# Optimization experiments

Hardware: AMD Instinct MI355X
Metric: run time of the kernel (lower is better)

Reference implementation:

```python
import jax, jax.numpy as jnp
import numpy as np

H = 64    # n_hidden
N = 1535  # input nodes; total graph nodes Nn = N + 1
B = 32    # batch
BN_EPS = 1e-5


def _p(key, shape, scale=0.05):
    return (jax.random.normal(key, shape, dtype=jnp.float32) * scale)


def setup_inputs() -> dict:
    key = jax.random.key(0)
    ks = jax.random.split(key, 32)
    inp = {
        'input_xx': jax.random.normal(ks[0], (B, N, 8), dtype=jnp.float32),
        'input_yy': jax.random.normal(ks[1], (B, N), dtype=jnp.float32),
        'output_xx': jax.random.normal(ks[2], (B, 1, 8), dtype=jnp.float32),
        # fc1: Linear(9, H); fc2: Linear(H, H)
        'W1': _p(ks[3], (H, 9)), 'b1': _p(ks[4], (H,)),
        'W2': _p(ks[5], (H, H)), 'b2': _p(ks[6], (H,)),
        # enc_new_x: Linear(8, H)
        'Wenc': _p(ks[7], (H, 8)), 'benc': _p(ks[8], (H,)),
        # Q, K, V: Linear(H, H)
        'WQ': _p(ks[9], (H, H)), 'bQ': _p(ks[10], (H,)),
        'WK': _p(ks[11], (H, H)), 'bK': _p(ks[12], (H,)),
        'WV': _p(ks[13], (H, H)), 'bV': _p(ks[14], (H,)),
        # QK: Linear(2H, 1) split into the q-half and k-half of its weight row
        'wQKq': _p(ks[15], (H,)), 'wQKk': _p(ks[16], (H,)),
        'bQK': _p(ks[17], ()),
        # A2N: Linear(H, H)
        'WA': _p(ks[18], (H, H)), 'bA': _p(ks[19], (H,)),
        # BatchNorm1d affine params
        'gamma': jnp.ones((H,), jnp.float32), 'beta': jnp.zeros((H,), jnp.float32),
        # heads
        'Wmu': _p(ks[20], (1, H)), 'bmu': _p(ks[21], (1,)),
        'Wsig': _p(ks[22], (1, H)), 'bsig': _p(ks[23], (1,)),
    }
    return inp


def _forward(input_xx, input_yy, output_xx, W1, b1, W2, b2, Wenc, benc,
             WQ, bQ, WK, bK, WV, bV, wQKq, wQKk, bQK, WA, bA,
             gamma, beta, Wmu, bmu, Wsig, bsig):
    # encode input nodes: cat(x, y) -> fc1 -> relu -> fc2 -> relu
    x = jnp.concatenate([input_xx, input_yy[..., None]], axis=-1)  # [B,N,9]
    h = jax.nn.relu(x @ W1.T + b1)
    h = jax.nn.relu(h @ W2.T + b2)                                  # [B,N,H]
    out_enc = jax.nn.relu(output_xx[:, 0, :] @ Wenc.T + benc)       # [B,H]
    # nodes: [Nn, B, H]  (node axis first, matching the torch list of nodes)
    nodes = jnp.concatenate([jnp.transpose(h, (1, 0, 2)), out_enc[None]], axis=0)

    def communicate(nodes):
        q = nodes @ WQ.T + bQ  # [Nn,B,H]
        k = nodes @ WK.T + bK
        v = nodes @ WV.T + bV
        # QK(cat(q,k)) decomposes additively: score[i,b,j] = q[i,b].wq + k[j,b].wk + b
        sq = q @ wQKq          # [Nn,B]
        sk = k @ wQKk          # [Nn,B]
        scores = sq[:, :, None] + sk.T[None, :, :] + bQK  # [Nn,B,Nn]
        w_att = jax.nn.softmax(scores, axis=-1)
        aggre = jnp.einsum('ibj,jbh->ibh', w_att, v)      # [Nn,B,H]
        z = aggre @ WA.T + bA
        # BatchNorm1d in training mode, applied per node over the batch axis
        mu = jnp.mean(z, axis=1, keepdims=True)
        var = jnp.var(z, axis=1, keepdims=True)
        z = (z - mu) / jnp.sqrt(var + BN_EPS) * gamma + beta
        return jax.nn.relu(z)

    for _ in range(4):
        nodes = communicate(nodes)

    agg = jnp.max(nodes, axis=0)                # [B,H]
    mu_out = agg @ Wmu.T + bmu                  # [B,1]
    sig_out = (agg @ Wsig.T + bsig) ** 2 + 0.01 # [B,1]
    return mu_out, sig_out


def reference(input_xx, input_yy, output_xx, W1, b1, W2, b2, Wenc, benc,
              WQ, bQ, WK, bK, WV, bV, wQKq, wQKk, bQK, WA, bA,
              gamma, beta, Wmu, bmu, Wsig, bsig):
    return _forward(input_xx, input_yy, output_xx, W1, b1, W2, b2, Wenc, benc,
                    WQ, bQ, WK, bK, WV, bV, wQKq, wQKk, bQK, WA, bA,
                    gamma, beta, Wmu, bmu, Wsig, bsig)
```

## Files before the change

kernel.cpp:

```cpp
#include <hip/hip_runtime.h>
#include <math.h>

#define HD    64
#define NIN   1535
#define NN    1536
#define BB    32
#define BN_EPS 1e-5f
#define CH    64
#define NCH   24

#define WS_M  0
#define WS_S  768
#define WS_V  1536

__global__ __launch_bounds__(256) void k_main(
    const float* __restrict__ xx,
    const float* __restrict__ yy,
    const float* __restrict__ oxx,
    const float* __restrict__ W1, const float* __restrict__ b1,
    const float* __restrict__ W2, const float* __restrict__ b2,
    const float* __restrict__ Wenc, const float* __restrict__ benc,
    const float* __restrict__ WK, const float* __restrict__ wQKk,
    float* __restrict__ ws) {
  __shared__ float W1s[576];
  __shared__ float b1s[64], b2s[64], bencs[64], us[64];
  __shared__ float Wencs[512];
  __shared__ float W2Ts[64 * 65];
  __shared__ float xs[512];
  __shared__ float ys[64];
  __shared__ float h1s[4][64];
  __shared__ float h2s[64 * 64];
  __shared__ float sks[64], e_s[64], rbuf[256], red0[1];

  const int t = threadIdx.x;
  const int blk = blockIdx.x;
  const int b = blk & 31;
  const int c = blk >> 5;
  const int pp = b * NCH + c;

  for (int e = t; e < 576; e += 256) W1s[e] = W1[e];
  for (int e = t; e < 512; e += 256) Wencs[e] = Wenc[e];
  for (int e = t; e < 4096; e += 256) {
    int h = e >> 6, k = e & 63;
    W2Ts[k * 65 + h] = W2[e];
  }
  for (int e = t; e < 512; e += 256) {
    int j = e >> 3, k = e & 7;
    int r0 = c * CH + j;
    xs[e] = (r0 < NIN) ? xx[(size_t)b * (NIN * 8) + (size_t)r0 * 8 + k]
                       : oxx[b * 8 + k];
  }
  if (t < 64) {
    b1s[t] = b1[t]; b2s[t] = b2[t]; bencs[t] = benc[t];
    int r0 = c * CH + t;
    ys[t] = (r0 < NIN) ? yy[b * NIN + r0] : 0.f;
    float a = 0.f;
    #pragma unroll
    for (int h0 = 0; h0 < 64; h0++) a += wQKk[h0] * WK[h0 * 64 + t];
    us[t] = a;
  }
  __syncthreads();

  const int w = t >> 6, lane = t & 63;
  float* h1w = h1s[w];

  float w2r[64];
  #pragma unroll
  for (int k = 0; k < 64; k++) w2r[k] = W2Ts[k * 65 + lane];

  for (int rr = 0; rr < 16; rr++) {
    int j = w * 16 + rr;
    int r0 = c * CH + j;
    const float* xr = xs + j * 8;
    float h2;
    if (r0 < NIN) {
      const float* wr = W1s + lane * 9;
      float a = b1s[lane];
      a += xr[0] * wr[0] + xr[1] * wr[1] + xr[2] * wr[2] + xr[3] * wr[3];
      a += xr[4] * wr[4] + xr[5] * wr[5] + xr[6] * wr[6] + xr[7] * wr[7];
      a += ys[j] * wr[8];
      h1w[lane] = fmaxf(a, 0.f);
      float a0 = b2s[lane], a1 = 0.f;
      #pragma unroll
      for (int k = 0; k < 64; k += 4) {
        float4 hv = *(const float4*)(h1w + k);
        a0 += hv.x * w2r[k]     + hv.z * w2r[k + 2];
        a1 += hv.y * w2r[k + 1] + hv.w * w2r[k + 3];
      }
      h2 = fmaxf(a0 + a1, 0.f);
    } else {
      const float* wr = Wencs + lane * 8;
      float a = bencs[lane];
      #pragma unroll
      for (int k = 0; k < 8; k++) a += xr[k] * wr[k];
      h2 = fmaxf(a, 0.f);
    }
    h2s[j * 64 + lane] = h2;
    float p = h2 * us[lane];
    p += __shfl_down(p, 32); p += __shfl_down(p, 16); p += __shfl_down(p, 8);
    p += __shfl_down(p, 4);  p += __shfl_down(p, 2);  p += __shfl_down(p, 1);
    if (lane == 0) sks[j] = p;
  }
  __syncthreads();

  if (t < 64) {
    float m = sks[t];
    m = fmaxf(m, __shfl_down(m, 32)); m = fmaxf(m, __shfl_down(m, 16));
    m = fmaxf(m, __shfl_down(m, 8));  m = fmaxf(m, __shfl_down(m, 4));
    m = fmaxf(m, __shfl_down(m, 2));  m = fmaxf(m, __shfl_down(m, 1));
    if (t == 0) red0[0] = m;
  }
  __syncthreads();
  float M = red0[0];
  if (t < 64) {
    float e = expf(sks[t] - M);
    e_s[t] = e;
    float s = e;
    s += __shfl_down(s, 32); s += __shfl_down(s, 16); s += __shfl_down(s, 8);
    s += __shfl_down(s, 4);  s += __shfl_down(s, 2);  s += __shfl_down(s, 1);
    if (t == 0) { ws[WS_M + pp] = M; ws[WS_S + pp] = s; }
  }
  __syncthreads();
  {
    float acc = 0.f;
    for (int j = w; j < 64; j += 4) acc += e_s[j] * h2s[j * 64 + lane];
    rbuf[t] = acc;
    __syncthreads();
    if (t < 64)
      ws[WS_V + pp * 64 + t] =
          rbuf[t] + rbuf[64 + t] + rbuf[128 + t] + rbuf[192 + t];
  }
}

__global__ __launch_bounds__(256) void k_tail(
    const float* __restrict__ ws,
    const float* __restrict__ WV, const float* __restrict__ bV,
    const float* __restrict__ WA, const float* __restrict__ bA,
    const float* __restrict__ gamma, const float* __restrict__ beta,
    const float* __restrict__ Wmu, const float* __restrict__ bmu,
    const float* __restrict__ Wsig, const float* __restrict__ bsig,
    float* __restrict__ out) {
  __shared__ float WAs[64 * 65];
  __shared__ float WVs[4096];
  __shared__ float WAVT[4096];
  __shared__ float bAVs[64];
  __shared__ float Ml[768], Sl[768], wexp[768];
  __shared__ float Mb[32], iSb[32];
  __shared__ float st[32 * 66];
  __shared__ float zs[32 * 66];
  __shared__ float scs[64], shs[64];
  const int t = threadIdx.x;

  for (int e = t; e < 4096; e += 256) {
    int h = e >> 6, m = e & 63;
    WAs[h * 65 + m] = WA[e];
    WVs[e] = WV[e];
  }
  for (int p = t; p < 768; p += 256) {
    Ml[p] = ws[WS_M + p];
    Sl[p] = ws[WS_S + p];
  }
  __syncthreads();

  if (t < 64) {
    float a = bA[t];
    #pragma unroll
    for (int k = 0; k < 64; k++) a += WAs[t * 65 + k] * bV[k];
    bAVs[t] = a;
  }
  {
    int kg = t >> 6, h = t & 63;
    float acc[16];
    #pragma unroll
    for (int kk = 0; kk < 16; kk++) acc[kk] = 0.f;
    for (int m = 0; m < 64; m++) {
      float wa = WAs[h * 65 + m];
      const float4* wv = (const float4*)(WVs + m * 64 + kg * 16);
      float4 w0 = wv[0], w1 = wv[1], w2 = wv[2], w3 = wv[3];
      acc[0]  += wa * w0.x; acc[1]  += wa * w0.y; acc[2]  += wa * w0.z; acc[3]  += wa * w0.w;
      acc[4]  += wa * w1.x; acc[5]  += wa * w1.y; acc[6]  += wa * w1.z; acc[7]  += wa * w1.w;
      acc[8]  += wa * w2.x; acc[9]  += wa * w2.y; acc[10] += wa * w2.z; acc[11] += wa * w2.w;
      acc[12] += wa * w3.x; acc[13] += wa * w3.y; acc[14] += wa * w3.z; acc[15] += wa * w3.w;
    }
    #pragma unroll
    for (int kk = 0; kk < 16; kk++) WAVT[(kg * 16 + kk) * 64 + h] = acc[kk];
  }
  if (t < 32) {
    float m = -1e30f;
    for (int cc = 0; cc < NCH; cc++) m = fmaxf(m, Ml[t * NCH + cc]);
    Mb[t] = m;
  }
  __syncthreads();
  for (int p = t; p < 768; p += 256) {
    int bb = p / NCH;
    wexp[p] = expf(Ml[p] - Mb[bb]);
  }
  __syncthreads();
  if (t < 32) {
    float s = 0.f;
    for (int cc = 0; cc < NCH; cc++) {
      int p = t * NCH + cc;
      s += Sl[p] * wexp[p];
    }
    iSb[t] = 1.0f / s;
  }
  __syncthreads();
  {
    int bb = t >> 3, hg = t & 7;
    float acc[8];
    #pragma unroll
    for (int jj = 0; jj < 8; jj++) acc[jj] = 0.f;
    for (int cc = 0; cc < NCH; cc++) {
      int p = bb * NCH + cc;
      float wgt = wexp[p];
      const float* vp = ws + WS_V + p * 64 + hg;
      #pragma unroll
      for (int jj = 0; jj < 8; jj++) acc[jj] += wgt * vp[jj * 8];
    }
    float is = iSb[bb];
    #pragma unroll
    for (int jj = 0; jj < 8; jj++) st[bb * 66 + hg + 8 * jj] = acc[jj] * is;
  }
  __syncthreads();

  for (int r = 0; r < 4; r++) {
    {
      int bb = t >> 3, hg = t & 7;
      float acc[8];
      #pragma unroll
      for (int jj = 0; jj < 8; jj++) acc[jj] = bAVs[hg + 8 * jj];
      for (int k = 0; k < 64; k++) {
        float v = st[bb * 66 + k];
        const float* wp = WAVT + k * 64 + hg;
        #pragma unroll
        for (int jj = 0; jj < 8; jj++) acc[jj] += v * wp[8 * jj];
      }
      #pragma unroll
      for (int jj = 0; jj < 8; jj++) zs[bb * 66 + hg + 8 * jj] = acc[jj];
    }
    __syncthreads();
    if (t < 64) {
      float s1 = 0.f;
      for (int bb2 = 0; bb2 < BB; bb2++) s1 += zs[bb2 * 66 + t];
      float mu = s1 * (1.0f / BB);
      float s2 = 0.f;
      for (int bb2 = 0; bb2 < BB; bb2++) {
        float d = zs[bb2 * 66 + t] - mu;
        s2 += d * d;
      }
      float inv = gamma[t] / sqrtf(s2 * (1.0f / BB) + BN_EPS);
      scs[t] = inv;
      shs[t] = beta[t] - mu * inv;
    }
    __syncthreads();
    for (int e = t; e < BB * 64; e += 256) {
      int bb2 = e >> 6, hh = e & 63;
      st[bb2 * 66 + hh] = fmaxf(zs[bb2 * 66 + hh] * scs[hh] + shs[hh], 0.f);
    }
    __syncthreads();
  }

  if (t < BB) {
    const float* nr = st + t * 66;
    float m = bmu[0], sg = bsig[0];
    #pragma unroll 8
    for (int h = 0; h < 64; h++) {
      float v = nr[h];
      m += v * Wmu[h];
      sg += v * Wsig[h];
    }
    out[t] = m;
    out[BB + t] = sg * sg + 0.01f;
  }
}

extern "C" void kernel_launch(void* const* d_in, const int* in_sizes, int n_in,
                              void* d_out, int out_size, void* d_ws, size_t ws_size,
                              hipStream_t stream) {
  const float* xx   = (const float*)d_in[0];
  const float* yy   = (const float*)d_in[1];
  const float* oxx  = (const float*)d_in[2];
  const float* W1   = (const float*)d_in[3];
  const float* b1   = (const float*)d_in[4];
  const float* W2   = (const float*)d_in[5];
  const float* b2   = (const float*)d_in[6];
  const float* Wenc = (const float*)d_in[7];
  const float* benc = (const float*)d_in[8];
  const float* WK   = (const float*)d_in[11];
  const float* WV   = (const float*)d_in[13];
  const float* bV   = (const float*)d_in[14];
  const float* wQKk = (const float*)d_in[16];
  const float* WA   = (const float*)d_in[18];
  const float* bA   = (const float*)d_in[19];
  const float* gamma= (const float*)d_in[20];
  const float* beta = (const float*)d_in[21];
  const float* Wmu  = (const float*)d_in[22];
  const float* bmu  = (const float*)d_in[23];
  const float* Wsig = (const float*)d_in[24];
  const float* bsig = (const float*)d_in[25];

  float* ws  = (float*)d_ws;
  float* out = (float*)d_out;

  k_main<<<BB * NCH, 256, 0, stream>>>(xx, yy, oxx, W1, b1, W2, b2, Wenc, benc,
                                       WK, wQKk, ws);
  k_tail<<<1, 256, 0, stream>>>(ws, WV, bV, WA, bA, gamma, beta,
                                Wmu, bmu, Wsig, bsig, out);
}
```

Before: 148.6 us.

## Split single-block tail into parallel combine kernel and wider final kernel

The single-block tail kernel is split in two. A 33-block kernel merges the per-chunk softmax partials for each batch in parallel, with one block precomputing the fused WA·WV matrix and bias. A 1024-thread final kernel then runs the four BN rounds with less work per thread. This targets the serial tail latency of one 256-thread block, at the cost of an extra kernel launch and a round trip through global memory.

```diff
diff --git a/kernel.cpp b/kernel.cpp
--- a/kernel.cpp
+++ b/kernel.cpp
@@ -9,9 +9,12 @@
 #define CH    64
 #define NCH   24
 
-#define WS_M  0
-#define WS_S  768
-#define WS_V  1536
+#define WS_M     0
+#define WS_S     768
+#define WS_V     1536
+#define WS_SS    50688
+#define WS_WAVT  52736
+#define WS_BAV   56832
 
 __global__ __launch_bounds__(256) void k_main(
     const float* __restrict__ xx,
@@ -132,43 +135,30 @@
   }
 }
 
-__global__ __launch_bounds__(256) void k_tail(
-    const float* __restrict__ ws,
+__global__ __launch_bounds__(256) void k_comb(
     const float* __restrict__ WV, const float* __restrict__ bV,
     const float* __restrict__ WA, const float* __restrict__ bA,
-    const float* __restrict__ gamma, const float* __restrict__ beta,
-    const float* __restrict__ Wmu, const float* __restrict__ bmu,
-    const float* __restrict__ Wsig, const float* __restrict__ bsig,
-    float* __restrict__ out) {
+    float* __restrict__ ws) {
   __shared__ float WAs[64 * 65];
   __shared__ float WVs[4096];
-  __shared__ float WAVT[4096];
-  __shared__ float bAVs[64];
-  __shared__ float Ml[768], Sl[768], wexp[768];
-  __shared__ float Mb[32], iSb[32];
-  __shared__ float st[32 * 66];
-  __shared__ float zs[32 * 66];
-  __shared__ float scs[64], shs[64];
+  __shared__ float Ml[NCH], Sl[NCH], wexp[NCH];
+  __shared__ float red[256];
+  __shared__ float MbS, iSbS;
   const int t = threadIdx.x;
 
-  for (int e = t; e < 4096; e += 256) {
-    int h = e >> 6, m = e & 63;
-    WAs[h * 65 + m] = WA[e];
-    WVs[e] = WV[e];
-  }
-  for (int p = t; p < 768; p += 256) {
-    Ml[p] = ws[WS_M + p];
-    Sl[p] = ws[WS_S + p];
-  }
-  __syncthreads();
-
-  if (t < 64) {
-    float a = bA[t];
-    #pragma unroll
-    for (int k = 0; k < 64; k++) a += WAs[t * 65 + k] * bV[k];
-    bAVs[t] = a;
-  }
-  {
+  if (blockIdx.x == 32) {
+    for (int e = t; e < 4096; e += 256) {
+      int h = e >> 6, m = e & 63;
+      WAs[h * 65 + m] = WA[e];
+      WVs[e] = WV[e];
+    }
+    __syncthreads();
+    if (t < 64) {
+      float a = bA[t];
+      #pragma unroll
+      for (int k = 0; k < 64; k++) a += WAs[t * 65 + k] * bV[k];
+      ws[WS_BAV + t] = a;
+    }
     int kg = t >> 6, h = t & 63;
     float acc[16];
     #pragma unroll
@@ -183,77 +173,103 @@
       acc[12] += wa * w3.x; acc[13] += wa * w3.y; acc[14] += wa * w3.z; acc[15] += wa * w3.w;
     }
     #pragma unroll
-    for (int kk = 0; kk < 16; kk++) WAVT[(kg * 16 + kk) * 64 + h] = acc[kk];
-  }
-  if (t < 32) {
+    for (int kk = 0; kk < 16; kk++) ws[WS_WAVT + (kg * 16 + kk) * 64 + h] = acc[kk];
+    return;
+  }
+
+  const int bb = blockIdx.x;
+  if (t < NCH) {
+    Ml[t] = ws[WS_M + bb * NCH + t];
+    Sl[t] = ws[WS_S + bb * NCH + t];
+  }
+  __syncthreads();
+  if (t == 0) {
     float m = -1e30f;
-    for (int cc = 0; cc < NCH; cc++) m = fmaxf(m, Ml[t * NCH + cc]);
-    Mb[t] = m;
-  }
-  __syncthreads();
-  for (int p = t; p < 768; p += 256) {
-    int bb = p / NCH;
-    wexp[p] = expf(Ml[p] - Mb[bb]);
-  }
-  __syncthreads();
-  if (t < 32) {
+    for (int cc = 0; cc < NCH; cc++) m = fmaxf(m, Ml[cc]);
+    MbS = m;
+  }
+  __syncthreads();
+  if (t < NCH) wexp[t] = expf(Ml[t] - MbS);
+  __syncthreads();
+  if (t == 0) {
     float s = 0.f;
-    for (int cc = 0; cc < NCH; cc++) {
-      int p = t * NCH + cc;
-      s += Sl[p] * wexp[p];
-    }
-    iSb[t] = 1.0f / s;
+    for (int cc = 0; cc < NCH; cc++) s += Sl[cc] * wexp[cc];
+    iSbS = 1.0f / s;
   }
   __syncthreads();
   {
-    int bb = t >> 3, hg = t & 7;
-    float acc[8];
-    #pragma unroll
-    for (int jj = 0; jj < 8; jj++) acc[jj] = 0.f;
-    for (int cc = 0; cc < NCH; cc++) {
-      int p = bb * NCH + cc;
-      float wgt = wexp[p];
-      const float* vp = ws + WS_V + p * 64 + hg;
-      #pragma unroll
-      for (int jj = 0; jj < 8; jj++) acc[jj] += wgt * vp[jj * 8];
-    }
-    float is = iSb[bb];
-    #pragma unroll
-    for (int jj = 0; jj < 8; jj++) st[bb * 66 + hg + 8 * jj] = acc[jj] * is;
+    int cg = t >> 6, h = t & 63;
+    float acc = 0.f;
+    for (int cc = cg; cc < NCH; cc += 4)
+      acc += wexp[cc] * ws[WS_V + (size_t)(bb * NCH + cc) * 64 + h];
+    red[t] = acc;
+    __syncthreads();
+    if (t < 64)
+      ws[WS_SS + bb * 64 + t] =
+          (red[t] + red[64 + t] + red[128 + t] + red[192 + t]) * iSbS;
+  }
+}
+
+__global__ __launch_bounds__(1024) void k_fin(
+    const float* __restrict__ ws,
+    const float* __restrict__ gamma, const float* __restrict__ beta,
+    const float* __restrict__ Wmu, const float* __restrict__ bmu,
+    const float* __restrict__ Wsig, const float* __restrict__ bsig,
+    float* __restrict__ out) {
+  __shared__ float WAVT[4096];
+  __shared__ float bAVs[64];
+  __shared__ float st[32 * 66];
+  __shared__ float zs[32 * 66];
+  __shared__ float scs[64], shs[64];
+  __shared__ float gammas[64], betas[64], wmus[64], wsigs[64];
+  const int t = threadIdx.x;
+
+  for (int e = t; e < 4096; e += 1024) WAVT[e] = ws[WS_WAVT + e];
+  if (t >= 1024 - 64) {
+    int h = t - (1024 - 64);
+    bAVs[h]   = ws[WS_BAV + h];
+    gammas[h] = gamma[h];
+    betas[h]  = beta[h];
+    wmus[h]   = Wmu[h];
+    wsigs[h]  = Wsig[h];
+  }
+  for (int e = t; e < 2048; e += 1024) {
+    int bb = e >> 6, hh = e & 63;
+    st[bb * 66 + hh] = ws[WS_SS + e];
   }
   __syncthreads();
 
   for (int r = 0; r < 4; r++) {
     {
-      int bb = t >> 3, hg = t & 7;
-      float acc[8];
-      #pragma unroll
-      for (int jj = 0; jj < 8; jj++) acc[jj] = bAVs[hg + 8 * jj];
+      int bb = t >> 5, hg = t & 31;
+      float a0 = bAVs[hg], a1 = bAVs[hg + 32];
+      #pragma unroll 16
       for (int k = 0; k < 64; k++) {
         float v = st[bb * 66 + k];
-        const float* wp = WAVT + k * 64 + hg;
-        #pragma unroll
-        for (int jj = 0; jj < 8; jj++) acc[jj] += v * wp[8 * jj];
+        a0 += v * WAVT[k * 64 + hg];
+        a1 += v * WAVT[k * 64 + hg + 32];
       }
-      #pragma unroll
-      for (int jj = 0; jj < 8; jj++) zs[bb * 66 + hg + 8 * jj] = acc[jj];
+      zs[bb * 66 + hg]      = a0;
+      zs[bb * 66 + hg + 32] = a1;
     }
     __syncthreads();
     if (t < 64) {
       float s1 = 0.f;
+      #pragma unroll
       for (int bb2 = 0; bb2 < BB; bb2++) s1 += zs[bb2 * 66 + t];
       float mu = s1 * (1.0f / BB);
       float s2 = 0.f;
+      #pragma unroll
       for (int bb2 = 0; bb2 < BB; bb2++) {
         float d = zs[bb2 * 66 + t] - mu;
         s2 += d * d;
       }
-      float inv = gamma[t] / sqrtf(s2 * (1.0f / BB) + BN_EPS);
+      float inv = gammas[t] / sqrtf(s2 * (1.0f / BB) + BN_EPS);
       scs[t] = inv;
-      shs[t] = beta[t] - mu * inv;
-    }
-    __syncthreads();
-    for (int e = t; e < BB * 64; e += 256) {
+      shs[t] = betas[t] - mu * inv;
+    }
+    __syncthreads();
+    for (int e = t; e < BB * 64; e += 1024) {
       int bb2 = e >> 6, hh = e & 63;
       st[bb2 * 66 + hh] = fmaxf(zs[bb2 * 66 + hh] * scs[hh] + shs[hh], 0.f);
     }
@@ -266,8 +282,8 @@
     #pragma unroll 8
     for (int h = 0; h < 64; h++) {
       float v = nr[h];
-      m += v * Wmu[h];
-      sg += v * Wsig[h];
+      m += v * wmus[h];
+      sg += v * wsigs[h];
     }
     out[t] = m;
     out[BB + t] = sg * sg + 0.01f;
@@ -304,6 +320,6 @@
 
   k_main<<<BB * NCH, 256, 0, stream>>>(xx, yy, oxx, W1, b1, W2, b2, Wenc, benc,
                                        WK, wQKk, ws);
-  k_tail<<<1, 256, 0, stream>>>(ws, WV, bV, WA, bA, gamma, beta,
-                                Wmu, bmu, Wsig, bsig, out);
+  k_comb<<<33, 256, 0, stream>>>(WV, bV, WA, bA, ws);
+  k_fin<<<1, 1024, 0, stream>>>(ws, gamma, beta, Wmu, bmu, Wsig, bsig, out);
 }
```

Measured after the change: 145.8 us. No clear change (-1.8%).

## Widen single-block tail kernel to 1024 threads and overlap its setup phases

Applied to the files above, without the earlier changes.

Relaunches the one-block tail kernel with 1024 threads. Half the threads fold WA·WV while the other half run the per-batch softmax combine in registers, instead of several serially synchronized phases. Each thread keeps a column of the folded weight matrix in registers for the four BN rounds and reads activations with vector loads. The final heads use wave shuffles. The aim is to shorten the latency-bound serial tail, at the cost of higher register pressure at 1024 threads.

```diff
diff --git a/kernel.cpp b/kernel.cpp
--- a/kernel.cpp
+++ b/kernel.cpp
@@ -9,9 +9,9 @@
 #define CH    64
 #define NCH   24
 
-#define WS_M  0
-#define WS_S  768
-#define WS_V  1536
+#define WS_M     0
+#define WS_S     768
+#define WS_V     1536
 
 __global__ __launch_bounds__(256) void k_main(
     const float* __restrict__ xx,
@@ -132,7 +132,8 @@
   }
 }
 
-__global__ __launch_bounds__(256) void k_tail(
+#define STS 68
+__global__ __launch_bounds__(1024) void k_post(
     const float* __restrict__ ws,
     const float* __restrict__ WV, const float* __restrict__ bV,
     const float* __restrict__ WA, const float* __restrict__ bA,
@@ -143,134 +144,136 @@
   __shared__ float WAs[64 * 65];
   __shared__ float WVs[4096];
   __shared__ float WAVT[4096];
-  __shared__ float bAVs[64];
-  __shared__ float Ml[768], Sl[768], wexp[768];
-  __shared__ float Mb[32], iSb[32];
-  __shared__ float st[32 * 66];
-  __shared__ float zs[32 * 66];
-  __shared__ float scs[64], shs[64];
+  __shared__ float Ml[768], Sl[768];
+  __shared__ float st[32 * STS], zs[32 * STS];
+  __shared__ float bAVs[64], scs[64], shs[64];
+  __shared__ float gammas[64], betas[64], wmus[64], wsigs[64], bVs[64];
   const int t = threadIdx.x;
 
-  for (int e = t; e < 4096; e += 256) {
+  for (int e = t; e < 4096; e += 1024) {
     int h = e >> 6, m = e & 63;
     WAs[h * 65 + m] = WA[e];
     WVs[e] = WV[e];
   }
-  for (int p = t; p < 768; p += 256) {
+  for (int p = t; p < 768; p += 1024) {
     Ml[p] = ws[WS_M + p];
     Sl[p] = ws[WS_S + p];
   }
-  __syncthreads();
-
   if (t < 64) {
-    float a = bA[t];
-    #pragma unroll
-    for (int k = 0; k < 64; k++) a += WAs[t * 65 + k] * bV[k];
-    bAVs[t] = a;
-  }
-  {
-    int kg = t >> 6, h = t & 63;
-    float acc[16];
-    #pragma unroll
-    for (int kk = 0; kk < 16; kk++) acc[kk] = 0.f;
+    gammas[t] = gamma[t]; betas[t] = beta[t];
+    wmus[t] = Wmu[t]; wsigs[t] = Wsig[t]; bVs[t] = bV[t];
+  }
+  __syncthreads();
+
+  if (t >= 512) {
+    int w2 = t - 512;
+    int kg = w2 >> 6;
+    int h  = w2 & 63;
+    float acc[8];
+    #pragma unroll
+    for (int j = 0; j < 8; j++) acc[j] = 0.f;
     for (int m = 0; m < 64; m++) {
       float wa = WAs[h * 65 + m];
-      const float4* wv = (const float4*)(WVs + m * 64 + kg * 16);
-      float4 w0 = wv[0], w1 = wv[1], w2 = wv[2], w3 = wv[3];
-      acc[0]  += wa * w0.x; acc[1]  += wa * w0.y; acc[2]  += wa * w0.z; acc[3]  += wa * w0.w;
-      acc[4]  += wa * w1.x; acc[5]  += wa * w1.y; acc[6]  += wa * w1.z; acc[7]  += wa * w1.w;
-      acc[8]  += wa * w2.x; acc[9]  += wa * w2.y; acc[10] += wa * w2.z; acc[11] += wa * w2.w;
-      acc[12] += wa * w3.x; acc[13] += wa * w3.y; acc[14] += wa * w3.z; acc[15] += wa * w3.w;
-    }
-    #pragma unroll
-    for (int kk = 0; kk < 16; kk++) WAVT[(kg * 16 + kk) * 64 + h] = acc[kk];
-  }
-  if (t < 32) {
-    float m = -1e30f;
-    for (int cc = 0; cc < NCH; cc++) m = fmaxf(m, Ml[t * NCH + cc]);
-    Mb[t] = m;
-  }
-  __syncthreads();
-  for (int p = t; p < 768; p += 256) {
-    int bb = p / NCH;
-    wexp[p] = expf(Ml[p] - Mb[bb]);
-  }
-  __syncthreads();
-  if (t < 32) {
-    float s = 0.f;
+      const float4* wv = (const float4*)(WVs + m * 64 + kg * 8);
+      float4 w0 = wv[0], w1 = wv[1];
+      acc[0] += wa * w0.x; acc[1] += wa * w0.y; acc[2] += wa * w0.z; acc[3] += wa * w0.w;
+      acc[4] += wa * w1.x; acc[5] += wa * w1.y; acc[6] += wa * w1.z; acc[7] += wa * w1.w;
+    }
+    #pragma unroll
+    for (int j = 0; j < 8; j++) WAVT[(kg * 8 + j) * 64 + h] = acc[j];
+    if (w2 < 64) {
+      float a = bA[w2];
+      #pragma unroll
+      for (int k = 0; k < 64; k++) a += WAs[w2 * 65 + k] * bVs[k];
+      bAVs[w2] = a;
+    }
+  } else {
+    int b = t >> 4, i = t & 15;
+    const float* Mb_ = Ml + b * NCH;
+    const float* Sb_ = Sl + b * NCH;
+    float mb = -1e30f;
+    #pragma unroll
+    for (int cc = 0; cc < NCH; cc++) mb = fmaxf(mb, Mb_[cc]);
+    float we[NCH];
+    float ssum = 0.f;
+    #pragma unroll
     for (int cc = 0; cc < NCH; cc++) {
-      int p = t * NCH + cc;
-      s += Sl[p] * wexp[p];
-    }
-    iSb[t] = 1.0f / s;
-  }
-  __syncthreads();
-  {
-    int bb = t >> 3, hg = t & 7;
-    float acc[8];
-    #pragma unroll
-    for (int jj = 0; jj < 8; jj++) acc[jj] = 0.f;
+      we[cc] = expf(Mb_[cc] - mb);
+      ssum += Sb_[cc] * we[cc];
+    }
+    float isb = 1.0f / ssum;
+    float a0 = 0.f, a1 = 0.f, a2 = 0.f, a3 = 0.f;
+    #pragma unroll 4
     for (int cc = 0; cc < NCH; cc++) {
-      int p = bb * NCH + cc;
-      float wgt = wexp[p];
-      const float* vp = ws + WS_V + p * 64 + hg;
-      #pragma unroll
-      for (int jj = 0; jj < 8; jj++) acc[jj] += wgt * vp[jj * 8];
-    }
-    float is = iSb[bb];
-    #pragma unroll
-    for (int jj = 0; jj < 8; jj++) st[bb * 66 + hg + 8 * jj] = acc[jj] * is;
-  }
-  __syncthreads();
+      const float* vp = ws + WS_V + (size_t)(b * NCH + cc) * 64 + i;
+      float wgt = we[cc];
+      a0 += wgt * vp[0];  a1 += wgt * vp[16];
+      a2 += wgt * vp[32]; a3 += wgt * vp[48];
+    }
+    st[b * STS + i]      = a0 * isb;
+    st[b * STS + i + 16] = a1 * isb;
+    st[b * STS + i + 32] = a2 * isb;
+    st[b * STS + i + 48] = a3 * isb;
+  }
+  __syncthreads();
+
+  const int bb = t >> 6;
+  const int hg = t & 63;
+  float wv_[64];
+  #pragma unroll
+  for (int k = 0; k < 64; k++) wv_[k] = WAVT[k * 64 + hg];
+  const float bav = bAVs[hg];
 
   for (int r = 0; r < 4; r++) {
-    {
-      int bb = t >> 3, hg = t & 7;
-      float acc[8];
-      #pragma unroll
-      for (int jj = 0; jj < 8; jj++) acc[jj] = bAVs[hg + 8 * jj];
-      for (int k = 0; k < 64; k++) {
-        float v = st[bb * 66 + k];
-        const float* wp = WAVT + k * 64 + hg;
-        #pragma unroll
-        for (int jj = 0; jj < 8; jj++) acc[jj] += v * wp[8 * jj];
-      }
-      #pragma unroll
-      for (int jj = 0; jj < 8; jj++) zs[bb * 66 + hg + 8 * jj] = acc[jj];
-    }
+    float a0 = bav, a1 = bav;
+    #pragma unroll
+    for (int k = 0; k < 64; k += 4) {
+      float4 v0 = *(const float4*)(st + bb * STS + k);
+      float4 v1 = *(const float4*)(st + (bb + 16) * STS + k);
+      a0 += v0.x * wv_[k] + v0.y * wv_[k + 1] + v0.z * wv_[k + 2] + v0.w * wv_[k + 3];
+      a1 += v1.x * wv_[k] + v1.y * wv_[k + 1] + v1.z * wv_[k + 2] + v1.w * wv_[k + 3];
+    }
+    zs[bb * STS + hg] = a0;
+    zs[(bb + 16) * STS + hg] = a1;
     __syncthreads();
     if (t < 64) {
       float s1 = 0.f;
-      for (int bb2 = 0; bb2 < BB; bb2++) s1 += zs[bb2 * 66 + t];
+      #pragma unroll
+      for (int b2 = 0; b2 < BB; b2++) s1 += zs[b2 * STS + t];
       float mu = s1 * (1.0f / BB);
       float s2 = 0.f;
-      for (int bb2 = 0; bb2 < BB; bb2++) {
-        float d = zs[bb2 * 66 + t] - mu;
+      #pragma unroll
+      for (int b2 = 0; b2 < BB; b2++) {
+        float d = zs[b2 * STS + t] - mu;
         s2 += d * d;
       }
-      float inv = gamma[t] / sqrtf(s2 * (1.0f / BB) + BN_EPS);
+      float inv = gammas[t] / sqrtf(s2 * (1.0f / BB) + BN_EPS);
       scs[t] = inv;
-      shs[t] = beta[t] - mu * inv;
+      shs[t] = betas[t] - mu * inv;
     }
     __syncthreads();
-    for (int e = t; e < BB * 64; e += 256) {
-      int bb2 = e >> 6, hh = e & 63;
-      st[bb2 * 66 + hh] = fmaxf(zs[bb2 * 66 + hh] * scs[hh] + shs[hh], 0.f);
+    for (int e = t; e < BB * 64; e += 1024) {
+      int b2 = e >> 6, hh = e & 63;
+      st[b2 * STS + hh] = fmaxf(zs[b2 * STS + hh] * scs[hh] + shs[hh], 0.f);
     }
     __syncthreads();
   }
 
-  if (t < BB) {
-    const float* nr = st + t * 66;
-    float m = bmu[0], sg = bsig[0];
-    #pragma unroll 8
-    for (int h = 0; h < 64; h++) {
-      float v = nr[h];
-      m += v * Wmu[h];
-      sg += v * Wsig[h];
-    }
-    out[t] = m;
-    out[BB + t] = sg * sg + 0.01f;
+  {
+    int b = t >> 5, i = t & 31;
+    float v0 = st[b * STS + i], v1 = st[b * STS + i + 32];
+    float pm = v0 * wmus[i] + v1 * wmus[i + 32];
+    float ps = v0 * wsigs[i] + v1 * wsigs[i + 32];
+    pm += __shfl_down(pm, 16); ps += __shfl_down(ps, 16);
+    pm += __shfl_down(pm, 8);  ps += __shfl_down(ps, 8);
+    pm += __shfl_down(pm, 4);  ps += __shfl_down(ps, 4);
+    pm += __shfl_down(pm, 2);  ps += __shfl_down(ps, 2);
+    pm += __shfl_down(pm, 1);  ps += __shfl_down(ps, 1);
+    if (i == 0) {
+      float sg = ps + bsig[0];
+      out[b] = pm + bmu[0];
+      out[BB + b] = sg * sg + 0.01f;
+    }
   }
 }
 
@@ -304,6 +307,6 @@
 
   k_main<<<BB * NCH, 256, 0, stream>>>(xx, yy, oxx, W1, b1, W2, b2, Wenc, benc,
                                        WK, wQKk, ws);
-  k_tail<<<1, 256, 0, stream>>>(ws, WV, bV, WA, bA, gamma, beta,
-                                Wmu, bmu, Wsig, bsig, out);
+  k_post<<<1, 1024, 0, stream>>>(ws, WV, bV, WA, bA, gamma, beta,
+                                 Wmu, bmu, Wsig, bsig, out);
 }
```

Measured after the change: 137.4 us. -7.5%, faster.

## Fuse producer and tail kernels into one launch with atomic-counter handoff

Applied to the files above, without the earlier changes.

Merges the two kernels into a single launch of 769 blocks. The 768 producer blocks each bump a global atomic counter when done, and the last block precomputes the WA·WV product and its bias while it spins on that counter before running the 4-round tail. This removes one launch boundary and overlaps the tail's weight setup with producer work. It also keeps the h2 rows in registers instead of shared memory and register-tiles the tail matmul. The cost is an extra memset per call and a spin-wait that relies on the tail block being scheduled alongside the producers, which risks deadlock if it takes residency the producers need.

```diff
diff --git a/kernel.cpp b/kernel.cpp
--- a/kernel.cpp
+++ b/kernel.cpp
@@ -8,12 +8,18 @@
 #define BN_EPS 1e-5f
 #define CH    64
 #define NCH   24
-
-#define WS_M  0
-#define WS_S  768
-#define WS_V  1536
-
-__global__ __launch_bounds__(256) void k_main(
+#define NPROD 768
+
+#define WS_M   0
+#define WS_S   768
+#define WS_V   1536
+#define CTR_F  50688
+
+#define STS 68
+
+#define SMEM_F 12480
+
+__global__ __launch_bounds__(256, 3) void k_all(
     const float* __restrict__ xx,
     const float* __restrict__ yy,
     const float* __restrict__ oxx,
@@ -21,153 +27,161 @@
     const float* __restrict__ W2, const float* __restrict__ b2,
     const float* __restrict__ Wenc, const float* __restrict__ benc,
     const float* __restrict__ WK, const float* __restrict__ wQKk,
-    float* __restrict__ ws) {
-  __shared__ float W1s[576];
-  __shared__ float b1s[64], b2s[64], bencs[64], us[64];
-  __shared__ float Wencs[512];
-  __shared__ float W2Ts[64 * 65];
-  __shared__ float xs[512];
-  __shared__ float ys[64];
-  __shared__ float h1s[4][64];
-  __shared__ float h2s[64 * 64];
-  __shared__ float sks[64], e_s[64], rbuf[256], red0[1];
-
-  const int t = threadIdx.x;
-  const int blk = blockIdx.x;
-  const int b = blk & 31;
-  const int c = blk >> 5;
-  const int pp = b * NCH + c;
-
-  for (int e = t; e < 576; e += 256) W1s[e] = W1[e];
-  for (int e = t; e < 512; e += 256) Wencs[e] = Wenc[e];
-  for (int e = t; e < 4096; e += 256) {
-    int h = e >> 6, k = e & 63;
-    W2Ts[k * 65 + h] = W2[e];
-  }
-  for (int e = t; e < 512; e += 256) {
-    int j = e >> 3, k = e & 7;
-    int r0 = c * CH + j;
-    xs[e] = (r0 < NIN) ? xx[(size_t)b * (NIN * 8) + (size_t)r0 * 8 + k]
-                       : oxx[b * 8 + k];
-  }
-  if (t < 64) {
-    b1s[t] = b1[t]; b2s[t] = b2[t]; bencs[t] = benc[t];
-    int r0 = c * CH + t;
-    ys[t] = (r0 < NIN) ? yy[b * NIN + r0] : 0.f;
-    float a = 0.f;
-    #pragma unroll
-    for (int h0 = 0; h0 < 64; h0++) a += wQKk[h0] * WK[h0 * 64 + t];
-    us[t] = a;
-  }
-  __syncthreads();
-
-  const int w = t >> 6, lane = t & 63;
-  float* h1w = h1s[w];
-
-  float w2r[64];
-  #pragma unroll
-  for (int k = 0; k < 64; k++) w2r[k] = W2Ts[k * 65 + lane];
-
-  for (int rr = 0; rr < 16; rr++) {
-    int j = w * 16 + rr;
-    int r0 = c * CH + j;
-    const float* xr = xs + j * 8;
-    float h2;
-    if (r0 < NIN) {
-      const float* wr = W1s + lane * 9;
-      float a = b1s[lane];
-      a += xr[0] * wr[0] + xr[1] * wr[1] + xr[2] * wr[2] + xr[3] * wr[3];
-      a += xr[4] * wr[4] + xr[5] * wr[5] + xr[6] * wr[6] + xr[7] * wr[7];
-      a += ys[j] * wr[8];
-      h1w[lane] = fmaxf(a, 0.f);
-      float a0 = b2s[lane], a1 = 0.f;
-      #pragma unroll
-      for (int k = 0; k < 64; k += 4) {
-        float4 hv = *(const float4*)(h1w + k);
-        a0 += hv.x * w2r[k]     + hv.z * w2r[k + 2];
-        a1 += hv.y * w2r[k + 1] + hv.w * w2r[k + 3];
-      }
-      h2 = fmaxf(a0 + a1, 0.f);
-    } else {
-      const float* wr = Wencs + lane * 8;
-      float a = bencs[lane];
-      #pragma unroll
-      for (int k = 0; k < 8; k++) a += xr[k] * wr[k];
-      h2 = fmaxf(a, 0.f);
-    }
-    h2s[j * 64 + lane] = h2;
-    float p = h2 * us[lane];
-    p += __shfl_down(p, 32); p += __shfl_down(p, 16); p += __shfl_down(p, 8);
-    p += __shfl_down(p, 4);  p += __shfl_down(p, 2);  p += __shfl_down(p, 1);
-    if (lane == 0) sks[j] = p;
-  }
-  __syncthreads();
-
-  if (t < 64) {
-    float m = sks[t];
-    m = fmaxf(m, __shfl_down(m, 32)); m = fmaxf(m, __shfl_down(m, 16));
-    m = fmaxf(m, __shfl_down(m, 8));  m = fmaxf(m, __shfl_down(m, 4));
-    m = fmaxf(m, __shfl_down(m, 2));  m = fmaxf(m, __shfl_down(m, 1));
-    if (t == 0) red0[0] = m;
-  }
-  __syncthreads();
-  float M = red0[0];
-  if (t < 64) {
-    float e = expf(sks[t] - M);
-    e_s[t] = e;
-    float s = e;
-    s += __shfl_down(s, 32); s += __shfl_down(s, 16); s += __shfl_down(s, 8);
-    s += __shfl_down(s, 4);  s += __shfl_down(s, 2);  s += __shfl_down(s, 1);
-    if (t == 0) { ws[WS_M + pp] = M; ws[WS_S + pp] = s; }
-  }
-  __syncthreads();
-  {
-    float acc = 0.f;
-    for (int j = w; j < 64; j += 4) acc += e_s[j] * h2s[j * 64 + lane];
-    rbuf[t] = acc;
-    __syncthreads();
-    if (t < 64)
-      ws[WS_V + pp * 64 + t] =
-          rbuf[t] + rbuf[64 + t] + rbuf[128 + t] + rbuf[192 + t];
-  }
-}
-
-__global__ __launch_bounds__(256) void k_tail(
-    const float* __restrict__ ws,
     const float* __restrict__ WV, const float* __restrict__ bV,
     const float* __restrict__ WA, const float* __restrict__ bA,
     const float* __restrict__ gamma, const float* __restrict__ beta,
     const float* __restrict__ Wmu, const float* __restrict__ bmu,
     const float* __restrict__ Wsig, const float* __restrict__ bsig,
-    float* __restrict__ out) {
-  __shared__ float WAs[64 * 65];
-  __shared__ float WVs[4096];
-  __shared__ float WAVT[4096];
-  __shared__ float bAVs[64];
-  __shared__ float Ml[768], Sl[768], wexp[768];
-  __shared__ float Mb[32], iSb[32];
-  __shared__ float st[32 * 66];
-  __shared__ float zs[32 * 66];
-  __shared__ float scs[64], shs[64];
+    float* __restrict__ ws, float* __restrict__ out) {
+  __shared__ float smem[SMEM_F];
   const int t = threadIdx.x;
+  const int blk = blockIdx.x;
+  int* ctr = (int*)(ws + CTR_F);
+
+  if (blk < NPROD) {
+    float* W1s   = smem;
+    float* Wencs = smem + 576;
+    float* b1s   = smem + 1088;
+    float* b2s   = smem + 1152;
+    float* bencs = smem + 1216;
+    float* us    = smem + 1280;
+    float* W2Ts  = smem + 1344;
+    float* xs    = smem + 5504;
+    float* ys    = smem + 6016;
+    float* h1s   = smem + 6080;
+    float* sks   = smem + 6336;
+    float* e_s   = smem + 6400;
+    float* rbuf  = smem + 6464;
+    float* red0  = smem + 6720;
+
+    const int b = blk & 31;
+    const int c = blk >> 5;
+    const int pp = b * NCH + c;
+
+    for (int e = t; e < 576; e += 256) W1s[e] = W1[e];
+    for (int e = t; e < 512; e += 256) Wencs[e] = Wenc[e];
+    for (int e = t; e < 4096; e += 256) {
+      int h = e >> 6, k = e & 63;
+      W2Ts[k * 65 + h] = W2[e];
+    }
+    for (int e = t; e < 512; e += 256) {
+      int j = e >> 3, k = e & 7;
+      int r0 = c * CH + j;
+      xs[e] = (r0 < NIN) ? xx[(size_t)b * (NIN * 8) + (size_t)r0 * 8 + k]
+                         : oxx[b * 8 + k];
+    }
+    if (t < 64) {
+      b1s[t] = b1[t]; b2s[t] = b2[t]; bencs[t] = benc[t];
+      int r0 = c * CH + t;
+      ys[t] = (r0 < NIN) ? yy[b * NIN + r0] : 0.f;
+      float a = 0.f;
+      #pragma unroll
+      for (int h0 = 0; h0 < 64; h0++) a += wQKk[h0] * WK[h0 * 64 + t];
+      us[t] = a;
+    }
+    __syncthreads();
+
+    const int w = t >> 6, lane = t & 63;
+    float* h1w = h1s + w * 64;
+
+    float w2r[64];
+    #pragma unroll
+    for (int k = 0; k < 64; k++) w2r[k] = W2Ts[k * 65 + lane];
+
+    float h2v[16];
+    #pragma unroll
+    for (int rr = 0; rr < 16; rr++) {
+      int j = w * 16 + rr;
+      int r0 = c * CH + j;
+      const float* xr = xs + j * 8;
+      float h2;
+      if (r0 < NIN) {
+        const float* wr = W1s + lane * 9;
+        float a = b1s[lane];
+        a += xr[0] * wr[0] + xr[1] * wr[1] + xr[2] * wr[2] + xr[3] * wr[3];
+        a += xr[4] * wr[4] + xr[5] * wr[5] + xr[6] * wr[6] + xr[7] * wr[7];
+        a += ys[j] * wr[8];
+        h1w[lane] = fmaxf(a, 0.f);
+        float a0 = b2s[lane], a1 = 0.f;
+        #pragma unroll
+        for (int k = 0; k < 64; k += 4) {
+          float4 hv = *(const float4*)(h1w + k);
+          a0 += hv.x * w2r[k]     + hv.z * w2r[k + 2];
+          a1 += hv.y * w2r[k + 1] + hv.w * w2r[k + 3];
+        }
+        h2 = fmaxf(a0 + a1, 0.f);
+      } else {
+        const float* wr = Wencs + lane * 8;
+        float a = bencs[lane];
+        #pragma unroll
+        for (int k = 0; k < 8; k++) a += xr[k] * wr[k];
+        h2 = fmaxf(a, 0.f);
+      }
+      h2v[rr] = h2;
+      float p = h2 * us[lane];
+      p += __shfl_down(p, 32); p += __shfl_down(p, 16); p += __shfl_down(p, 8);
+      p += __shfl_down(p, 4);  p += __shfl_down(p, 2);  p += __shfl_down(p, 1);
+      if (lane == 0) sks[j] = p;
+    }
+    __syncthreads();
+
+    if (t < 64) {
+      float m = sks[t];
+      m = fmaxf(m, __shfl_down(m, 32)); m = fmaxf(m, __shfl_down(m, 16));
+      m = fmaxf(m, __shfl_down(m, 8));  m = fmaxf(m, __shfl_down(m, 4));
+      m = fmaxf(m, __shfl_down(m, 2));  m = fmaxf(m, __shfl_down(m, 1));
+      if (t == 0) red0[0] = m;
+    }
+    __syncthreads();
+    float M = red0[0];
+    if (t < 64) {
+      float e = expf(sks[t] - M);
+      e_s[t] = e;
+      float s = e;
+      s += __shfl_down(s, 32); s += __shfl_down(s, 16); s += __shfl_down(s, 8);
+      s += __shfl_down(s, 4);  s += __shfl_down(s, 2);  s += __shfl_down(s, 1);
+      if (t == 0) { ws[WS_M + pp] = M; ws[WS_S + pp] = s; }
+    }
+    __syncthreads();
+    {
+      float acc = 0.f;
+      #pragma unroll
+      for (int rr = 0; rr < 16; rr++) acc += e_s[w * 16 + rr] * h2v[rr];
+      rbuf[t] = acc;
+      __syncthreads();
+      if (t < 64)
+        ws[WS_V + (size_t)pp * 64 + t] =
+            rbuf[t] + rbuf[64 + t] + rbuf[128 + t] + rbuf[192 + t];
+    }
+
+    __threadfence();
+    __syncthreads();
+    if (t == 0) atomicAdd(ctr, 1);
+    return;
+  }
+
+  float* WAs    = smem;
+  float* WVs    = smem + 4160;
+  float* WAVTl  = smem + 8256;
+  float* bVs    = smem + 12352;
+  float* bAVs   = smem + 12416;
+  float* st  = smem;
+  float* zs  = smem + 2176;
+  float* scs = smem + 4352;
+  float* shs = smem + 4416;
+  float* gam = smem + 4480;
+  float* bet = smem + 4544;
+  float* wmu = smem + 4608;
+  float* wsg = smem + 4672;
 
   for (int e = t; e < 4096; e += 256) {
     int h = e >> 6, m = e & 63;
     WAs[h * 65 + m] = WA[e];
     WVs[e] = WV[e];
   }
-  for (int p = t; p < 768; p += 256) {
-    Ml[p] = ws[WS_M + p];
-    Sl[p] = ws[WS_S + p];
-  }
+  if (t < 64) bVs[t] = bV[t];
   __syncthreads();
 
-  if (t < 64) {
-    float a = bA[t];
-    #pragma unroll
-    for (int k = 0; k < 64; k++) a += WAs[t * 65 + k] * bV[k];
-    bAVs[t] = a;
-  }
   {
     int kg = t >> 6, h = t & 63;
     float acc[16];
@@ -183,91 +197,116 @@
       acc[12] += wa * w3.x; acc[13] += wa * w3.y; acc[14] += wa * w3.z; acc[15] += wa * w3.w;
     }
     #pragma unroll
-    for (int kk = 0; kk < 16; kk++) WAVT[(kg * 16 + kk) * 64 + h] = acc[kk];
-  }
-  if (t < 32) {
-    float m = -1e30f;
-    for (int cc = 0; cc < NCH; cc++) m = fmaxf(m, Ml[t * NCH + cc]);
-    Mb[t] = m;
+    for (int kk = 0; kk < 16; kk++) WAVTl[(kg * 16 + kk) * 64 + h] = acc[kk];
+    if (t < 64) {
+      float a = bA[t];
+      #pragma unroll
+      for (int k = 0; k < 64; k++) a += WAs[t * 65 + k] * bVs[k];
+      bAVs[t] = a;
+    }
+  }
+
+  if (t == 0) {
+    while (__hip_atomic_load(ctr, __ATOMIC_RELAXED, __HIP_MEMORY_SCOPE_AGENT)
+           < NPROD) {
+      __builtin_amdgcn_s_sleep(8);
+    }
   }
   __syncthreads();
-  for (int p = t; p < 768; p += 256) {
-    int bb = p / NCH;
-    wexp[p] = expf(Ml[p] - Mb[bb]);
+  __threadfence();
+
+  const int hg = t & 63;
+  float wv_[64];
+  #pragma unroll
+  for (int k = 0; k < 64; k++) wv_[k] = WAVTl[k * 64 + hg];
+  const float bav = bAVs[hg];
+  if (t < 64) {
+    gam[t] = gamma[t]; bet[t] = beta[t];
+    wmu[t] = Wmu[t];   wsg[t] = Wsig[t];
+  }
+
+  {
+    int b2 = t >> 3, i = t & 7;
+    const float* Mb_ = ws + WS_M + b2 * NCH;
+    const float* Sb_ = ws + WS_S + b2 * NCH;
+    float mb = -1e30f;
+    #pragma unroll
+    for (int cc = 0; cc < NCH; cc++) mb = fmaxf(mb, Mb_[cc]);
+    float we[NCH];
+    float ssum = 0.f;
+    #pragma unroll
+    for (int cc = 0; cc < NCH; cc++) {
+      we[cc] = expf(Mb_[cc] - mb);
+      ssum += Sb_[cc] * we[cc];
+    }
+    float isb = 1.0f / ssum;
+    float a0 = 0.f, a1 = 0.f, a2 = 0.f, a3 = 0.f;
+    float a4 = 0.f, a5 = 0.f, a6 = 0.f, a7 = 0.f;
+    #pragma unroll
+    for (int cc = 0; cc < NCH; cc++) {
+      const float4* vp =
+          (const float4*)(ws + WS_V + (size_t)(b2 * NCH + cc) * 64 + i * 8);
+      float4 v0 = vp[0], v1 = vp[1];
+      float wgt = we[cc];
+      a0 += wgt * v0.x; a1 += wgt * v0.y; a2 += wgt * v0.z; a3 += wgt * v0.w;
+      a4 += wgt * v1.x; a5 += wgt * v1.y; a6 += wgt * v1.z; a7 += wgt * v1.w;
+    }
+    float* sr = st + b2 * STS + i * 8;
+    sr[0] = a0 * isb; sr[1] = a1 * isb; sr[2] = a2 * isb; sr[3] = a3 * isb;
+    sr[4] = a4 * isb; sr[5] = a5 * isb; sr[6] = a6 * isb; sr[7] = a7 * isb;
   }
   __syncthreads();
-  if (t < 32) {
-    float s = 0.f;
-    for (int cc = 0; cc < NCH; cc++) {
-      int p = t * NCH + cc;
-      s += Sl[p] * wexp[p];
-    }
-    iSb[t] = 1.0f / s;
-  }
-  __syncthreads();
-  {
-    int bb = t >> 3, hg = t & 7;
-    float acc[8];
-    #pragma unroll
-    for (int jj = 0; jj < 8; jj++) acc[jj] = 0.f;
-    for (int cc = 0; cc < NCH; cc++) {
-      int p = bb * NCH + cc;
-      float wgt = wexp[p];
-      const float* vp = ws + WS_V + p * 64 + hg;
-      #pragma unroll
-      for (int jj = 0; jj < 8; jj++) acc[jj] += wgt * vp[jj * 8];
-    }
-    float is = iSb[bb];
-    #pragma unroll
-    for (int jj = 0; jj < 8; jj++) st[bb * 66 + hg + 8 * jj] = acc[jj] * is;
-  }
-  __syncthreads();
-
+
+  const int w0 = t >> 6;
   for (int r = 0; r < 4; r++) {
     {
-      int bb = t >> 3, hg = t & 7;
-      float acc[8];
-      #pragma unroll
-      for (int jj = 0; jj < 8; jj++) acc[jj] = bAVs[hg + 8 * jj];
-      for (int k = 0; k < 64; k++) {
-        float v = st[bb * 66 + k];
-        const float* wp = WAVT + k * 64 + hg;
+      float a[8];
+      #pragma unroll
+      for (int j = 0; j < 8; j++) a[j] = bav;
+      #pragma unroll
+      for (int k = 0; k < 64; k += 4) {
         #pragma unroll
-        for (int jj = 0; jj < 8; jj++) acc[jj] += v * wp[8 * jj];
+        for (int j = 0; j < 8; j++) {
+          float4 v = *(const float4*)(st + (w0 * 8 + j) * STS + k);
+          a[j] += v.x * wv_[k]     + v.y * wv_[k + 1] +
+                  v.z * wv_[k + 2] + v.w * wv_[k + 3];
+        }
       }
       #pragma unroll
-      for (int jj = 0; jj < 8; jj++) zs[bb * 66 + hg + 8 * jj] = acc[jj];
+      for (int j = 0; j < 8; j++) zs[(w0 * 8 + j) * STS + hg] = a[j];
     }
     __syncthreads();
     if (t < 64) {
       float s1 = 0.f;
-      for (int bb2 = 0; bb2 < BB; bb2++) s1 += zs[bb2 * 66 + t];
+      #pragma unroll
+      for (int b2 = 0; b2 < BB; b2++) s1 += zs[b2 * STS + t];
       float mu = s1 * (1.0f / BB);
       float s2 = 0.f;
-      for (int bb2 = 0; bb2 < BB; bb2++) {
-        float d = zs[bb2 * 66 + t] - mu;
+      #pragma unroll
+      for (int b2 = 0; b2 < BB; b2++) {
+        float d = zs[b2 * STS + t] - mu;
         s2 += d * d;
       }
-      float inv = gamma[t] / sqrtf(s2 * (1.0f / BB) + BN_EPS);
+      float inv = gam[t] / sqrtf(s2 * (1.0f / BB) + BN_EPS);
       scs[t] = inv;
-      shs[t] = beta[t] - mu * inv;
+      shs[t] = bet[t] - mu * inv;
     }
     __syncthreads();
     for (int e = t; e < BB * 64; e += 256) {
-      int bb2 = e >> 6, hh = e & 63;
-      st[bb2 * 66 + hh] = fmaxf(zs[bb2 * 66 + hh] * scs[hh] + shs[hh], 0.f);
+      int b2 = e >> 6, hh = e & 63;
+      st[b2 * STS + hh] = fmaxf(zs[b2 * STS + hh] * scs[hh] + shs[hh], 0.f);
     }
     __syncthreads();
   }
 
   if (t < BB) {
-    const float* nr = st + t * 66;
+    const float* nr = st + t * STS;
     float m = bmu[0], sg = bsig[0];
     #pragma unroll 8
     for (int h = 0; h < 64; h++) {
       float v = nr[h];
-      m += v * Wmu[h];
-      sg += v * Wsig[h];
+      m += v * wmu[h];
+      sg += v * wsg[h];
     }
     out[t] = m;
     out[BB + t] = sg * sg + 0.01f;
@@ -302,8 +341,9 @@
   float* ws  = (float*)d_ws;
   float* out = (float*)d_out;
 
-  k_main<<<BB * NCH, 256, 0, stream>>>(xx, yy, oxx, W1, b1, W2, b2, Wenc, benc,
-                                       WK, wQKk, ws);
-  k_tail<<<1, 256, 0, stream>>>(ws, WV, bV, WA, bA, gamma, beta,
-                                Wmu, bmu, Wsig, bsig, out);
+  hipMemsetAsync((char*)d_ws + (size_t)CTR_F * 4, 0, 4, stream);
+
+  k_all<<<NPROD + 1, 256, 0, stream>>>(
+      xx, yy, oxx, W1, b1, W2, b2, Wenc, benc, WK, wQKk,
+      WV, bV, WA, bA, gamma, beta, Wmu, bmu, Wsig, bsig, ws, out);
 }
```

Result: slower. 203.2 us (+36.8%).
